# Performance work log

Hardware: AMD Instinct MI355X
Metric: run time of the kernel (lower is better)

## Reference

```python
import jax, jax.numpy as jnp
import numpy as np
from jax import lax

HORIZON = 333.0
LAM = 0.95
DISCOUNT = 1.0 - 1.0 / HORIZON  # contdisc=False

B, T, D, H = 1024, 65, 512, 512


def _mlp(x, W1, b1, W2, b2, W3, b3):
    # x: [B, T, D] -> scalar critic mean per step [B, T]
    h = jax.nn.silu(jnp.einsum('btd,dh->bth', x, W1) + b1)
    h = jax.nn.silu(jnp.einsum('bth,hk->btk', h, W2) + b2)
    out = jnp.einsum('bth,ho->bto', h, W3) + b3
    return out[..., 0]


def setup_inputs() -> dict:
    key = jax.random.key(0)
    ks = jax.random.split(key, 8)
    s = 1.0 / np.sqrt(D)
    sh = 1.0 / np.sqrt(H)
    return {
        'feat': jax.random.normal(ks[0], (B, T, D), jnp.float32),
        'reward': jax.random.normal(ks[1], (B, T), jnp.float32) * 0.1,
        'cont': jnp.ones((B, T), jnp.float32),
        'voffset': jnp.zeros((1,), jnp.float32),
        'vscale': jnp.ones((1,), jnp.float32),
        'W1n': jax.random.normal(ks[2], (D, H), jnp.float32) * s,
        'b1n': jnp.zeros((H,), jnp.float32),
        'W2n': jax.random.normal(ks[3], (H, H), jnp.float32) * sh,
        'b2n': jnp.zeros((H,), jnp.float32),
        'W3n': jax.random.normal(ks[4], (H, 1), jnp.float32) * sh,
        'b3n': jnp.zeros((1,), jnp.float32),
        'W1s': jax.random.normal(ks[5], (D, H), jnp.float32) * s,
        'b1s': jnp.zeros((H,), jnp.float32),
        'W2s': jax.random.normal(ks[6], (H, H), jnp.float32) * sh,
        'b2s': jnp.zeros((H,), jnp.float32),
        'W3s': jax.random.normal(ks[7], (H, 1), jnp.float32) * sh,
        'b3s': jnp.zeros((1,), jnp.float32),
    }


def reference(feat, reward, cont, voffset, vscale,
              W1n, b1n, W2n, b2n, W3n, b3n,
              W1s, b1s, W2s, b2s, W3s, b3s):
    critic = _mlp(feat, W1n, b1n, W2n, b2n, W3n, b3n)        # [B, T]
    slowcritic = _mlp(feat, W1s, b1s, W2s, b2s, W3s, b3s)    # [B, T]
    val = critic * vscale + voffset
    slowval = slowcritic * vscale + voffset
    tarval = slowval  # config.agent.slowtar = True

    disc = cont[:, 1:] * DISCOUNT                             # [B, T-1]
    interm = reward[:, 1:] + (1.0 - LAM) * disc * tarval[:, 1:]
    boot = tarval[:, -1]                                      # [B]

    # reversed linear recurrence r_t = interm_t + disc_t*lam*r_{t+1}
    xs = (jnp.moveaxis(interm, 1, 0), jnp.moveaxis(disc, 1, 0))  # [T-1, B]

    def step(carry, x):
        i_t, d_t = x
        r = i_t + d_t * LAM * carry
        return r, r

    _, ys = lax.scan(step, boot, xs, reverse=True)            # [T-1, B], time order t=0..T-2
    ret = jnp.moveaxis(ys, 0, 1)                              # [B, T-1]
    return ret
```

## Files before the change

### kernel.cpp

```cpp
#include <hip/hip_runtime.h>
#include <stdint.h>


#define MROWS 66560
#define RBLK 520
#define LAMF 0.95f
#define DISCF ((float)(1.0 - 1.0 / 333.0))

typedef __attribute__((ext_vector_type(8))) __bf16 bf16x8;
typedef __attribute__((ext_vector_type(4))) float f32x4;
typedef __attribute__((ext_vector_type(4))) unsigned int u32x4;

__device__ __forceinline__ unsigned short f2bf(float f) {
  unsigned int u = __float_as_uint(f);
  return (unsigned short)((u + 0x7FFFu + ((u >> 16) & 1u)) >> 16);
}
__device__ __forceinline__ float silu_f(float x) { return x / (1.0f + __expf(-x)); }

__device__ __forceinline__ void gload_lds16(const void* g, void* l) {
  __builtin_amdgcn_global_load_lds(
      (const __attribute__((address_space(1))) void*)g,
      (__attribute__((address_space(3))) void*)l, 16, 0, 0);
}

__global__ __launch_bounds__(256) void prep_kernel(
    const float* __restrict__ W1, const float* __restrict__ W2,
    unsigned short* __restrict__ Wt1, unsigned short* __restrict__ Wt2,
    float* __restrict__ tarval) {
  int id = blockIdx.x * 256 + threadIdx.x;
  int n = id >> 9, k = id & 511;
  Wt1[id] = f2bf(W1[k * 512 + n]);
  Wt2[id] = f2bf(W2[k * 512 + n]);
  if (id < MROWS) tarval[id] = 0.0f;
}

__device__ __forceinline__ void tile_map(int bid, int& rb, int& cb) {
  int xcd = bid & 7;
  int idx = bid >> 3;
  rb = xcd * 65 + (idx >> 2);
  cb = idx & 3;
}

__global__ __launch_bounds__(256) void gemm1_kernel(
    const float* __restrict__ A, const unsigned short* __restrict__ Bt,
    const float* __restrict__ bias, unsigned short* __restrict__ Hout) {
  __shared__ __align__(16) unsigned char lds[2 * 128 * 64 * 2];
  unsigned char* Alds = lds;
  unsigned char* Blds = lds + 128 * 64 * 2;

  int rb, cb; tile_map(blockIdx.x, rb, cb);
  const int m0 = rb * 128, n0 = cb * 128;
  const int tid = threadIdx.x;
  const int lane = tid & 63, w = tid >> 6;
  const int wr = w >> 1, wc = w & 1;

  f32x4 acc[4][4] = {};

  for (int ks = 0; ks < 512; ks += 64) {
    {
      const int base = w * 1024;
#pragma unroll
      for (int i = 0; i < 4; ++i) {
        int L = i * 4096 + base + lane * 16;
        int row = L >> 7, kb = L & 127;
        gload_lds16((const void*)(Bt + (size_t)(n0 + row) * 512 + ks + (kb >> 1)),
                    (void*)(Blds + i * 4096 + base));
      }
    }
#pragma unroll
    for (int i = 0; i < 4; ++i) {
      int L = (i * 256 + tid) * 16;
      int row = L >> 7, kb = L & 127;
      const float* src = A + (size_t)(m0 + row) * 512 + ks + (kb >> 1);
      f32x4 v0 = *(const f32x4*)(src);
      f32x4 v1 = *(const f32x4*)(src + 4);
      union { unsigned short h[8]; u32x4 u; } p;
      p.h[0] = f2bf(v0[0]); p.h[1] = f2bf(v0[1]); p.h[2] = f2bf(v0[2]); p.h[3] = f2bf(v0[3]);
      p.h[4] = f2bf(v1[0]); p.h[5] = f2bf(v1[1]); p.h[6] = f2bf(v1[2]); p.h[7] = f2bf(v1[3]);
      *(u32x4*)(Alds + L) = p.u;
    }
    __syncthreads();
#pragma unroll
    for (int kk = 0; kk < 2; ++kk) {
      bf16x8 af[4], bf[4];
      const int kbyte = kk * 64 + ((lane >> 4) * 16);
#pragma unroll
      for (int m = 0; m < 4; ++m)
        af[m] = *(const bf16x8*)(Alds + (wr * 64 + m * 16 + (lane & 15)) * 128 + kbyte);
#pragma unroll
      for (int n = 0; n < 4; ++n)
        bf[n] = *(const bf16x8*)(Blds + (wc * 64 + n * 16 + (lane & 15)) * 128 + kbyte);
#pragma unroll
      for (int m = 0; m < 4; ++m)
#pragma unroll
        for (int n = 0; n < 4; ++n)
          acc[m][n] = __builtin_amdgcn_mfma_f32_16x16x32_bf16(af[m], bf[n], acc[m][n], 0, 0, 0);
    }
    __syncthreads();
  }
#pragma unroll
  for (int n = 0; n < 4; ++n) {
    const int col = n0 + wc * 64 + n * 16 + (lane & 15);
    const float bn = bias[col];
#pragma unroll
    for (int m = 0; m < 4; ++m) {
      const int rbase = m0 + wr * 64 + m * 16 + (lane >> 4) * 4;
#pragma unroll
      for (int i = 0; i < 4; ++i)
        Hout[(size_t)(rbase + i) * 512 + col] = f2bf(silu_f(acc[m][n][i] + bn));
    }
  }
}

__global__ __launch_bounds__(256) void gemm2_kernel(
    const unsigned short* __restrict__ A, const unsigned short* __restrict__ Bt,
    const float* __restrict__ bias, const float* __restrict__ W3,
    float* __restrict__ tarval) {
  __shared__ __align__(16) unsigned char lds[2 * 128 * 64 * 2];
  unsigned char* Alds = lds;
  unsigned char* Blds = lds + 128 * 64 * 2;

  int rb, cb; tile_map(blockIdx.x, rb, cb);
  const int m0 = rb * 128, n0 = cb * 128;
  const int tid = threadIdx.x;
  const int lane = tid & 63, w = tid >> 6;
  const int wr = w >> 1, wc = w & 1;

  f32x4 acc[4][4] = {};

  for (int ks = 0; ks < 512; ks += 64) {
    const int base = w * 1024;
#pragma unroll
    for (int i = 0; i < 4; ++i) {
      int L = i * 4096 + base + lane * 16;
      int row = L >> 7, kb = L & 127;
      gload_lds16((const void*)(A + (size_t)(m0 + row) * 512 + ks + (kb >> 1)),
                  (void*)(Alds + i * 4096 + base));
    }
#pragma unroll
    for (int i = 0; i < 4; ++i) {
      int L = i * 4096 + base + lane * 16;
      int row = L >> 7, kb = L & 127;
      gload_lds16((const void*)(Bt + (size_t)(n0 + row) * 512 + ks + (kb >> 1)),
                  (void*)(Blds + i * 4096 + base));
    }
    __syncthreads();
#pragma unroll
    for (int kk = 0; kk < 2; ++kk) {
      bf16x8 af[4], bf[4];
      const int kbyte = kk * 64 + ((lane >> 4) * 16);
#pragma unroll
      for (int m = 0; m < 4; ++m)
        af[m] = *(const bf16x8*)(Alds + (wr * 64 + m * 16 + (lane & 15)) * 128 + kbyte);
#pragma unroll
      for (int n = 0; n < 4; ++n)
        bf[n] = *(const bf16x8*)(Blds + (wc * 64 + n * 16 + (lane & 15)) * 128 + kbyte);
#pragma unroll
      for (int m = 0; m < 4; ++m)
#pragma unroll
        for (int n = 0; n < 4; ++n)
          acc[m][n] = __builtin_amdgcn_mfma_f32_16x16x32_bf16(af[m], bf[n], acc[m][n], 0, 0, 0);
    }
    __syncthreads();
  }
#pragma unroll
  for (int m = 0; m < 4; ++m) {
    float ps0 = 0.f, ps1 = 0.f, ps2 = 0.f, ps3 = 0.f;
#pragma unroll
    for (int n = 0; n < 4; ++n) {
      const int col = n0 + wc * 64 + n * 16 + (lane & 15);
      const float bn = bias[col];
      const float w3 = W3[col];
      ps0 += silu_f(acc[m][n][0] + bn) * w3;
      ps1 += silu_f(acc[m][n][1] + bn) * w3;
      ps2 += silu_f(acc[m][n][2] + bn) * w3;
      ps3 += silu_f(acc[m][n][3] + bn) * w3;
    }
    float ps[4] = {ps0, ps1, ps2, ps3};
#pragma unroll
    for (int i = 0; i < 4; ++i) {
      float v = ps[i];
      v += __shfl_xor(v, 1);
      v += __shfl_xor(v, 2);
      v += __shfl_xor(v, 4);
      v += __shfl_xor(v, 8);
      if ((lane & 15) == 0) {
        int row = m0 + wr * 64 + m * 16 + (lane >> 4) * 4 + i;
        atomicAdd(&tarval[row], v);
      }
    }
  }
}

__global__ __launch_bounds__(64) void scan_kernel(
    const float* __restrict__ tarval, const float* __restrict__ reward,
    const float* __restrict__ cont, const float* __restrict__ voffset,
    const float* __restrict__ vscale, const float* __restrict__ b3,
    float* __restrict__ out) {
  __shared__ float tv[64];
  __shared__ float ret[64];
  const int b = blockIdx.x, t = threadIdx.x;
  tv[t] = (tarval[b * 65 + 1 + t] + b3[0]) * vscale[0] + voffset[0];
  __syncthreads();
  if (t == 0) {
    float carry = tv[63];
    for (int j = 63; j >= 0; --j) {
      const int tt = j + 1;
      const float disc = cont[b * 65 + tt] * DISCF;
      const float r = reward[b * 65 + tt] + disc * ((1.0f - LAMF) * tv[j] + LAMF * carry);
      ret[j] = r;
      carry = r;
    }
  }
  __syncthreads();
  out[b * 64 + t] = ret[t];
}

extern "C" void kernel_launch(void* const* d_in, const int* in_sizes, int n_in,
                              void* d_out, int out_size, void* d_ws, size_t ws_size,
                              hipStream_t stream) {
  const float* feat    = (const float*)d_in[0];
  const float* reward  = (const float*)d_in[1];
  const float* cont    = (const float*)d_in[2];
  const float* voffset = (const float*)d_in[3];
  const float* vscale  = (const float*)d_in[4];
  const float* W1s = (const float*)d_in[11];
  const float* b1s = (const float*)d_in[12];
  const float* W2s = (const float*)d_in[13];
  const float* b2s = (const float*)d_in[14];
  const float* W3s = (const float*)d_in[15];
  const float* b3s = (const float*)d_in[16];

  char* ws = (char*)d_ws;
  unsigned short* Wt1 = (unsigned short*)ws;
  unsigned short* Wt2 = (unsigned short*)(ws + (512u << 10));
  float* tarval       = (float*)(ws + (1024u << 10));
  unsigned short* H1  = (unsigned short*)(ws + (2048u << 10));

  prep_kernel<<<1024, 256, 0, stream>>>(W1s, W2s, Wt1, Wt2, tarval);
  gemm1_kernel<<<RBLK * 4, 256, 0, stream>>>(feat, Wt1, b1s, H1);
  gemm2_kernel<<<RBLK * 4, 256, 0, stream>>>(H1, Wt2, b2s, W3s, tarval);
  scan_kernel<<<1024, 64, 0, stream>>>(tarval, reward, cont, voffset, vscale, b3s,
                                       (float*)d_out);
}
```

Before: 376.1 us.

## Load GEMM fragments directly from global memory and tile weight transpose

Both GEMM kernels drop the LDS staging and barriers and have each lane load its MFMA fragments straight from global memory into registers. Each wave now reads its own A and B rows, so the block no longer shares that data through LDS and redundant global/L2 traffic goes up. The prep kernel switches to an LDS-tiled transpose for coalesced weight reads and a smaller grid for zeroing tarval. The intent is to remove synchronisation and LDS round trips, at the risk of more uncoalesced, strided global loads.

```diff
diff --git a/kernel.cpp b/kernel.cpp
--- a/kernel.cpp
+++ b/kernel.cpp
@@ -9,29 +9,46 @@
 
 typedef __attribute__((ext_vector_type(8))) __bf16 bf16x8;
 typedef __attribute__((ext_vector_type(4))) float f32x4;
-typedef __attribute__((ext_vector_type(4))) unsigned int u32x4;
 
 __device__ __forceinline__ unsigned short f2bf(float f) {
   unsigned int u = __float_as_uint(f);
   return (unsigned short)((u + 0x7FFFu + ((u >> 16) & 1u)) >> 16);
 }
 __device__ __forceinline__ float silu_f(float x) { return x / (1.0f + __expf(-x)); }
-
-__device__ __forceinline__ void gload_lds16(const void* g, void* l) {
-  __builtin_amdgcn_global_load_lds(
-      (const __attribute__((address_space(1))) void*)g,
-      (__attribute__((address_space(3))) void*)l, 16, 0, 0);
-}
 
 __global__ __launch_bounds__(256) void prep_kernel(
     const float* __restrict__ W1, const float* __restrict__ W2,
     unsigned short* __restrict__ Wt1, unsigned short* __restrict__ Wt2,
     float* __restrict__ tarval) {
-  int id = blockIdx.x * 256 + threadIdx.x;
-  int n = id >> 9, k = id & 511;
-  Wt1[id] = f2bf(W1[k * 512 + n]);
-  Wt2[id] = f2bf(W2[k * 512 + n]);
-  if (id < MROWS) tarval[id] = 0.0f;
+  int b = blockIdx.x;
+  if (b < 128) {
+    const float* W = (b < 64) ? W1 : W2;
+    unsigned short* Wt = (b < 64) ? Wt1 : Wt2;
+    int tb = b & 63;
+    int tk = (tb >> 3) * 64;
+    int tn = (tb & 7) * 64;
+    __shared__ float tile[64][65];
+    int tx = threadIdx.x & 63;
+    int ty4 = threadIdx.x >> 6;
+#pragma unroll
+    for (int i = 0; i < 16; ++i) {
+      int row = ty4 * 16 + i;
+      tile[row][tx] = W[(size_t)(tk + row) * 512 + tn + tx];
+    }
+    __syncthreads();
+#pragma unroll
+    for (int i = 0; i < 16; ++i) {
+      int nrow = ty4 * 16 + i;
+      Wt[(size_t)(tn + nrow) * 512 + tk + tx] = f2bf(tile[tx][nrow]);
+    }
+  } else {
+    int id = (b - 128) * 256 + threadIdx.x;
+#pragma unroll
+    for (int i = 0; i < 17; ++i) {
+      int idx = id + i * 4096;
+      if (idx < MROWS) tarval[idx] = 0.0f;
+    }
+  }
 }
 
 __device__ __forceinline__ void tile_map(int bid, int& rb, int& cb) {
@@ -44,67 +61,51 @@
 __global__ __launch_bounds__(256) void gemm1_kernel(
     const float* __restrict__ A, const unsigned short* __restrict__ Bt,
     const float* __restrict__ bias, unsigned short* __restrict__ Hout) {
-  __shared__ __align__(16) unsigned char lds[2 * 128 * 64 * 2];
-  unsigned char* Alds = lds;
-  unsigned char* Blds = lds + 128 * 64 * 2;
-
   int rb, cb; tile_map(blockIdx.x, rb, cb);
   const int m0 = rb * 128, n0 = cb * 128;
-  const int tid = threadIdx.x;
-  const int lane = tid & 63, w = tid >> 6;
+  const int lane = threadIdx.x & 63, w = threadIdx.x >> 6;
   const int wr = w >> 1, wc = w & 1;
+  const int q = lane >> 4, r = lane & 15;
+
+  unsigned int aoff[4], boff[4];
+#pragma unroll
+  for (int m = 0; m < 4; ++m)
+    aoff[m] = (unsigned int)(m0 + wr * 64 + m * 16 + r) * 512u + q * 8u;
+#pragma unroll
+  for (int n = 0; n < 4; ++n)
+    boff[n] = (unsigned int)(n0 + wc * 64 + n * 16 + r) * 512u + q * 8u;
 
   f32x4 acc[4][4] = {};
 
-  for (int ks = 0; ks < 512; ks += 64) {
-    {
-      const int base = w * 1024;
-#pragma unroll
-      for (int i = 0; i < 4; ++i) {
-        int L = i * 4096 + base + lane * 16;
-        int row = L >> 7, kb = L & 127;
-        gload_lds16((const void*)(Bt + (size_t)(n0 + row) * 512 + ks + (kb >> 1)),
-                    (void*)(Blds + i * 4096 + base));
-      }
-    }
-#pragma unroll
-    for (int i = 0; i < 4; ++i) {
-      int L = (i * 256 + tid) * 16;
-      int row = L >> 7, kb = L & 127;
-      const float* src = A + (size_t)(m0 + row) * 512 + ks + (kb >> 1);
-      f32x4 v0 = *(const f32x4*)(src);
-      f32x4 v1 = *(const f32x4*)(src + 4);
-      union { unsigned short h[8]; u32x4 u; } p;
-      p.h[0] = f2bf(v0[0]); p.h[1] = f2bf(v0[1]); p.h[2] = f2bf(v0[2]); p.h[3] = f2bf(v0[3]);
-      p.h[4] = f2bf(v1[0]); p.h[5] = f2bf(v1[1]); p.h[6] = f2bf(v1[2]); p.h[7] = f2bf(v1[3]);
-      *(u32x4*)(Alds + L) = p.u;
-    }
-    __syncthreads();
-#pragma unroll
-    for (int kk = 0; kk < 2; ++kk) {
-      bf16x8 af[4], bf[4];
-      const int kbyte = kk * 64 + ((lane >> 4) * 16);
-#pragma unroll
-      for (int m = 0; m < 4; ++m)
-        af[m] = *(const bf16x8*)(Alds + (wr * 64 + m * 16 + (lane & 15)) * 128 + kbyte);
+#pragma unroll 4
+  for (int k0 = 0; k0 < 512; k0 += 32) {
+    bf16x8 af[4], bfr[4];
+#pragma unroll
+    for (int n = 0; n < 4; ++n)
+      bfr[n] = *(const bf16x8*)(Bt + boff[n] + k0);
+#pragma unroll
+    for (int m = 0; m < 4; ++m) {
+      f32x4 lo = *(const f32x4*)(A + aoff[m] + k0);
+      f32x4 hi = *(const f32x4*)(A + aoff[m] + k0 + 4);
+      af[m][0] = (__bf16)lo[0]; af[m][1] = (__bf16)lo[1];
+      af[m][2] = (__bf16)lo[2]; af[m][3] = (__bf16)lo[3];
+      af[m][4] = (__bf16)hi[0]; af[m][5] = (__bf16)hi[1];
+      af[m][6] = (__bf16)hi[2]; af[m][7] = (__bf16)hi[3];
+    }
+#pragma unroll
+    for (int m = 0; m < 4; ++m)
 #pragma unroll
       for (int n = 0; n < 4; ++n)
-        bf[n] = *(const bf16x8*)(Blds + (wc * 64 + n * 16 + (lane & 15)) * 128 + kbyte);
-#pragma unroll
-      for (int m = 0; m < 4; ++m)
-#pragma unroll
-        for (int n = 0; n < 4; ++n)
-          acc[m][n] = __builtin_amdgcn_mfma_f32_16x16x32_bf16(af[m], bf[n], acc[m][n], 0, 0, 0);
-    }
-    __syncthreads();
-  }
+        acc[m][n] = __builtin_amdgcn_mfma_f32_16x16x32_bf16(af[m], bfr[n], acc[m][n], 0, 0, 0);
+  }
+
 #pragma unroll
   for (int n = 0; n < 4; ++n) {
-    const int col = n0 + wc * 64 + n * 16 + (lane & 15);
+    const int col = n0 + wc * 64 + n * 16 + r;
     const float bn = bias[col];
 #pragma unroll
     for (int m = 0; m < 4; ++m) {
-      const int rbase = m0 + wr * 64 + m * 16 + (lane >> 4) * 4;
+      const int rbase = m0 + wr * 64 + m * 16 + q * 4;
 #pragma unroll
       for (int i = 0; i < 4; ++i)
         Hout[(size_t)(rbase + i) * 512 + col] = f2bf(silu_f(acc[m][n][i] + bn));
@@ -116,59 +117,44 @@
     const unsigned short* __restrict__ A, const unsigned short* __restrict__ Bt,
     const float* __restrict__ bias, const float* __restrict__ W3,
     float* __restrict__ tarval) {
-  __shared__ __align__(16) unsigned char lds[2 * 128 * 64 * 2];
-  unsigned char* Alds = lds;
-  unsigned char* Blds = lds + 128 * 64 * 2;
-
   int rb, cb; tile_map(blockIdx.x, rb, cb);
   const int m0 = rb * 128, n0 = cb * 128;
-  const int tid = threadIdx.x;
-  const int lane = tid & 63, w = tid >> 6;
+  const int lane = threadIdx.x & 63, w = threadIdx.x >> 6;
   const int wr = w >> 1, wc = w & 1;
+  const int q = lane >> 4, r = lane & 15;
+
+  unsigned int aoff[4], boff[4];
+#pragma unroll
+  for (int m = 0; m < 4; ++m)
+    aoff[m] = (unsigned int)(m0 + wr * 64 + m * 16 + r) * 512u + q * 8u;
+#pragma unroll
+  for (int n = 0; n < 4; ++n)
+    boff[n] = (unsigned int)(n0 + wc * 64 + n * 16 + r) * 512u + q * 8u;
 
   f32x4 acc[4][4] = {};
 
-  for (int ks = 0; ks < 512; ks += 64) {
-    const int base = w * 1024;
-#pragma unroll
-    for (int i = 0; i < 4; ++i) {
-      int L = i * 4096 + base + lane * 16;
-      int row = L >> 7, kb = L & 127;
-      gload_lds16((const void*)(A + (size_t)(m0 + row) * 512 + ks + (kb >> 1)),
-                  (void*)(Alds + i * 4096 + base));
-    }
-#pragma unroll
-    for (int i = 0; i < 4; ++i) {
-      int L = i * 4096 + base + lane * 16;
-      int row = L >> 7, kb = L & 127;
-      gload_lds16((const void*)(Bt + (size_t)(n0 + row) * 512 + ks + (kb >> 1)),
-                  (void*)(Blds + i * 4096 + base));
-    }
-    __syncthreads();
-#pragma unroll
-    for (int kk = 0; kk < 2; ++kk) {
-      bf16x8 af[4], bf[4];
-      const int kbyte = kk * 64 + ((lane >> 4) * 16);
-#pragma unroll
-      for (int m = 0; m < 4; ++m)
-        af[m] = *(const bf16x8*)(Alds + (wr * 64 + m * 16 + (lane & 15)) * 128 + kbyte);
+#pragma unroll 4
+  for (int k0 = 0; k0 < 512; k0 += 32) {
+    bf16x8 af[4], bfr[4];
+#pragma unroll
+    for (int m = 0; m < 4; ++m)
+      af[m] = *(const bf16x8*)(A + aoff[m] + k0);
+#pragma unroll
+    for (int n = 0; n < 4; ++n)
+      bfr[n] = *(const bf16x8*)(Bt + boff[n] + k0);
+#pragma unroll
+    for (int m = 0; m < 4; ++m)
 #pragma unroll
       for (int n = 0; n < 4; ++n)
-        bf[n] = *(const bf16x8*)(Blds + (wc * 64 + n * 16 + (lane & 15)) * 128 + kbyte);
-#pragma unroll
-      for (int m = 0; m < 4; ++m)
-#pragma unroll
-        for (int n = 0; n < 4; ++n)
-          acc[m][n] = __builtin_amdgcn_mfma_f32_16x16x32_bf16(af[m], bf[n], acc[m][n], 0, 0, 0);
-    }
-    __syncthreads();
-  }
+        acc[m][n] = __builtin_amdgcn_mfma_f32_16x16x32_bf16(af[m], bfr[n], acc[m][n], 0, 0, 0);
+  }
+
 #pragma unroll
   for (int m = 0; m < 4; ++m) {
     float ps0 = 0.f, ps1 = 0.f, ps2 = 0.f, ps3 = 0.f;
 #pragma unroll
     for (int n = 0; n < 4; ++n) {
-      const int col = n0 + wc * 64 + n * 16 + (lane & 15);
+      const int col = n0 + wc * 64 + n * 16 + r;
       const float bn = bias[col];
       const float w3 = W3[col];
       ps0 += silu_f(acc[m][n][0] + bn) * w3;
@@ -184,8 +170,8 @@
       v += __shfl_xor(v, 2);
       v += __shfl_xor(v, 4);
       v += __shfl_xor(v, 8);
-      if ((lane & 15) == 0) {
-        int row = m0 + wr * 64 + m * 16 + (lane >> 4) * 4 + i;
+      if (r == 0) {
+        int row = m0 + wr * 64 + m * 16 + q * 4 + i;
         atomicAdd(&tarval[row], v);
       }
     }
@@ -237,7 +223,7 @@
   float* tarval       = (float*)(ws + (1024u << 10));
   unsigned short* H1  = (unsigned short*)(ws + (2048u << 10));
 
-  prep_kernel<<<1024, 256, 0, stream>>>(W1s, W2s, Wt1, Wt2, tarval);
+  prep_kernel<<<144, 256, 0, stream>>>(W1s, W2s, Wt1, Wt2, tarval);
   gemm1_kernel<<<RBLK * 4, 256, 0, stream>>>(feat, Wt1, b1s, H1);
   gemm2_kernel<<<RBLK * 4, 256, 0, stream>>>(H1, Wt2, b2s, W3s, tarval);
   scan_kernel<<<1024, 64, 0, stream>>>(tarval, reward, cont, voffset, vscale, b3s,
```

Result: slower. 592.3 us (+57.5%).
